# Optimization experiments

Hardware: AMD Instinct MI355X
Metric: run time of the kernel (lower is better)

The kernel has to match this reference:

```python
import jax, jax.numpy as jnp
import numpy as np

NUM_HEADS = 8
NUM_GROUPS = 32
EPS = 1e-5


def group_norm(x, gamma, beta):
    # x: (B, C, N)
    B, C, N = x.shape
    xg = x.reshape(B, NUM_GROUPS, (C // NUM_GROUPS) * N)
    mean = xg.mean(axis=-1, keepdims=True)
    var = xg.var(axis=-1, keepdims=True)
    xg = (xg - mean) * jax.lax.rsqrt(var + EPS)
    x = xg.reshape(B, C, N)
    return x * gamma[None, :, None] + beta[None, :, None]


def setup_inputs() -> dict:
    key = jax.random.key(0)
    ks = jax.random.split(key, 7)
    B, C, H, W = 16, 512, 32, 32
    return {
        "x": jax.random.normal(ks[0], (B, C, H, W), dtype=jnp.float32),
        "gamma": jax.random.uniform(ks[1], (C,), dtype=jnp.float32, minval=0.5, maxval=1.5),
        "beta": jax.random.normal(ks[2], (C,), dtype=jnp.float32) * 0.1,
        "w_qkv": jax.random.normal(ks[3], (3 * C, C), dtype=jnp.float32) * 0.02,
        "b_qkv": jax.random.normal(ks[4], (3 * C,), dtype=jnp.float32) * 0.01,
        "w_proj": jax.random.normal(ks[5], (C, C), dtype=jnp.float32) * 0.02,
        "b_proj": jax.random.normal(ks[6], (C,), dtype=jnp.float32) * 0.01,
    }


def reference(x, gamma, beta, w_qkv, b_qkv, w_proj, b_proj):
    B, C, Hs, Ws = x.shape
    N = Hs * Ws
    x3 = x.reshape(B, C, N)
    xn = group_norm(x3, gamma, beta)
    # 1x1 Conv1d == channel-wise linear: (3C, C) x (B, C, N) -> (B, 3C, N)
    qkv = jnp.einsum('oc,bcn->bon', w_qkv, xn) + b_qkv[None, :, None]
    ch = C // NUM_HEADS
    qkv = qkv.reshape(B * NUM_HEADS, 3 * ch, N)
    q, k, v = jnp.split(qkv, 3, axis=1)  # each (B*H, ch, N)
    scale = ch ** (-0.25)
    w = jnp.einsum('bct,bcs->bts', q * scale, k * scale)  # (B*H, N, N)
    w = jax.nn.softmax(w.astype(jnp.float32), axis=-1).astype(q.dtype)
    h = jnp.einsum('bts,bcs->bct', w, v)  # (B*H, ch, N)
    h = h.reshape(B, C, N)
    h = jnp.einsum('oc,bcn->bon', w_proj, h) + b_proj[None, :, None]
    return (x3 + h).reshape(B, C, Hs, Ws)
```

## Files before the change

kernel.cpp:

```cpp
#include <hip/hip_runtime.h>
#include <stdint.h>

typedef unsigned short u16;
typedef float f32x4 __attribute__((ext_vector_type(4)));
typedef short bf16x8 __attribute__((ext_vector_type(8)));

#define DEV __device__ __forceinline__

DEV u16 f2bf(float f) {
  union { float f; unsigned int u; } v; v.f = f;
  unsigned int u = v.u;
  u = (u + 0x7FFFu + ((u >> 16) & 1u)) >> 16;
  return (u16)u;
}

DEV float exp2_(float x) {
#if __has_builtin(__builtin_amdgcn_exp2f)
  return __builtin_amdgcn_exp2f(x);
#else
  return exp2f(x);
#endif
}

DEV unsigned int cvt_pk_bf16(float lo, float hi) {
  unsigned int r;
  asm("v_cvt_pk_bf16_f32 %0, %1, %2" : "=v"(r) : "v"(lo), "v"(hi));
  return r;
}

typedef __attribute__((address_space(1))) const unsigned int* gas_t;
typedef __attribute__((address_space(3))) unsigned int* las_t;
DEV void gload16(const void* g, void* l) {
  __builtin_amdgcn_global_load_lds((gas_t)g, (las_t)l, 16, 0, 0);
}

DEV f32x4 zf4() { f32x4 z = {0.f, 0.f, 0.f, 0.f}; return z; }

static constexpr float QK_SCALE = 0.35355339059327373f;
static constexpr float LOG2E    = 1.4426950408889634f;

static constexpr size_t OFF_WQKV  = 0;
static constexpr size_t OFF_WPROJ = 1572864;
static constexpr size_t OFF_XNT   = 2097152;
static constexpr size_t OFF_Q     = 18874368;
static constexpr size_t OFF_K     = 35651584;
static constexpr size_t OFF_V     = 52428800;
static constexpr size_t OFF_HT    = 69206016;

__global__ __launch_bounds__(256) void wconv_kernel(const float* __restrict__ wqkv,
                                                    const float* __restrict__ wproj,
                                                    u16* __restrict__ dq, u16* __restrict__ dp) {
  int i = blockIdx.x * 256 + threadIdx.x;
  const float4* src; u16* dst; int j;
  if (i < 196608) { src = (const float4*)wqkv;  dst = dq; j = i; }
  else            { src = (const float4*)wproj; dst = dp; j = i - 196608; }
  float4 v = src[j];
  unsigned int lo = (unsigned int)f2bf(v.x) | ((unsigned int)f2bf(v.y) << 16);
  unsigned int hi = (unsigned int)f2bf(v.z) | ((unsigned int)f2bf(v.w) << 16);
  uint2 o; o.x = lo; o.y = hi;
  *(uint2*)(dst + (size_t)j * 4) = o;
}

__global__ __launch_bounds__(256, 4) void gn_fused_kernel(const float* __restrict__ x,
                                                          const float* __restrict__ gamma,
                                                          const float* __restrict__ beta,
                                                          u16* __restrict__ xnt) {
  __shared__ u16 Tls[16 * 1024];
  __shared__ float rs[4], rss[4], bcast[2];
  int grp = blockIdx.x;
  int b = grp >> 5, g = grp & 31;
  int tid = threadIdx.x;
  const float4* p = (const float4*)(x + (size_t)grp * 16384);
  float4 v[16];
  float s = 0.f, ss = 0.f;
  #pragma unroll
  for (int it = 0; it < 16; ++it) {
    v[it] = p[it * 256 + tid];
    s  += v[it].x + v[it].y + v[it].z + v[it].w;
    ss += v[it].x*v[it].x + v[it].y*v[it].y + v[it].z*v[it].z + v[it].w*v[it].w;
  }
  #pragma unroll
  for (int off = 32; off > 0; off >>= 1) {
    s  += __shfl_down(s, off);
    ss += __shfl_down(ss, off);
  }
  int wid = tid >> 6;
  if ((tid & 63) == 0) { rs[wid] = s; rss[wid] = ss; }
  __syncthreads();
  if (tid == 0) {
    s  = rs[0] + rs[1] + rs[2] + rs[3];
    ss = rss[0] + rss[1] + rss[2] + rss[3];
    float mean = s * (1.f / 16384.f);
    float var  = ss * (1.f / 16384.f) - mean * mean;
    bcast[0] = mean;
    bcast[1] = rsqrtf(var + 1e-5f);
  }
  __syncthreads();
  float mean = bcast[0], rstd = bcast[1];
  #pragma unroll
  for (int it = 0; it < 16; ++it) {
    int c = g*16 + it;
    float ga = gamma[c] * rstd, be = beta[c] - mean * ga;
    uint2 pk;
    pk.x = cvt_pk_bf16(v[it].x*ga + be, v[it].y*ga + be);
    pk.y = cvt_pk_bf16(v[it].z*ga + be, v[it].w*ga + be);
    *(uint2*)&Tls[it*1024 + tid*4] = pk;
  }
  __syncthreads();
  u16* dst = xnt + ((size_t)b * 1024) * 512 + g*16;
  for (int r = 0; r < 8; ++r) {
    int idx = r*256 + tid, n = idx >> 1, half = idx & 1;
    u16 tmp[8];
    #pragma unroll
    for (int cc = 0; cc < 8; ++cc) tmp[cc] = Tls[(half*8 + cc)*1024 + n];
    *(uint4*)(dst + (size_t)n*512 + half*8) = *(uint4*)tmp;
  }
}

template<int EPI>
__global__ __launch_bounds__(256) void gemm_kernel(const u16* __restrict__ A,
                                                   const u16* __restrict__ Bm,
                                                   const float* __restrict__ bias,
                                                   u16* __restrict__ Qp, u16* __restrict__ Kp,
                                                   u16* __restrict__ Vp,
                                                   const float* __restrict__ xres,
                                                   float* __restrict__ outp) {
  __shared__ u16 lds[4 * 128 * 64];
  int tid = threadIdx.x, lane = tid & 63, wid = tid >> 6;
  int tl = lane & 15, g = lane >> 4;
  int wm = wid >> 1, wn = wid & 1;
  int tM = blockIdx.y, tN = blockIdx.x;
  int o0 = tM * 128, n0 = tN * 128;
  f32x4 acc[4][4];
  #pragma unroll
  for (int i = 0; i < 4; ++i)
    #pragma unroll
    for (int j = 0; j < 4; ++j) acc[i][j] = zf4();

  int rl = lane >> 3, sg = lane & 7;
  const u16* Ag = A  + (size_t)(o0 + wid*32 + rl) * 512 + ((sg ^ rl) << 3);
  const u16* Bg = Bm + (size_t)(n0 + wid*32 + rl) * 512 + ((sg ^ rl) << 3);
  int wofs = wid*32*64;

#define STAGE_GEMM(buf, kt)                                                     \
  {                                                                             \
    u16* Ad = lds + (buf)*16384 + wofs;                                         \
    u16* Bd = lds + (buf)*16384 + 8192 + wofs;                                  \
    _Pragma("unroll")                                                           \
    for (int q = 0; q < 4; ++q) {                                               \
      gload16(Ag + (size_t)q*8*512 + (kt)*64, Ad + q*8*64);                     \
      gload16(Bg + (size_t)q*8*512 + (kt)*64, Bd + q*8*64);                     \
    }                                                                           \
  }

  STAGE_GEMM(0, 0);
  __syncthreads();
  for (int kt = 0; kt < 8; ++kt) {
    int cur = kt & 1;
    if (kt < 7) STAGE_GEMM(cur ^ 1, kt + 1);
    const u16* Als = lds + cur*16384;
    const u16* Bls = lds + cur*16384 + 8192;
    #pragma unroll
    for (int kk = 0; kk < 2; ++kk) {
      bf16x8 av[4], bv[4];
      #pragma unroll
      for (int mi = 0; mi < 4; ++mi)
        av[mi] = *(const bf16x8*)&Als[(wm*64 + mi*16 + tl)*64 + (((kk*4 + g) ^ (tl & 7)) << 3)];
      #pragma unroll
      for (int ni = 0; ni < 4; ++ni)
        bv[ni] = *(const bf16x8*)&Bls[(wn*64 + ni*16 + tl)*64 + (((kk*4 + g) ^ (tl & 7)) << 3)];
      #pragma unroll
      for (int mi = 0; mi < 4; ++mi)
        #pragma unroll
        for (int ni = 0; ni < 4; ++ni)
          acc[mi][ni] = __builtin_amdgcn_mfma_f32_16x16x32_bf16(av[mi], bv[ni], acc[mi][ni], 0, 0, 0);
    }
    __syncthreads();
  }
#undef STAGE_GEMM

  if (EPI == 1) {
    #pragma unroll
    for (int mi = 0; mi < 4; ++mi) {
      int mb = mi*16 + (g << 2);
      float4 bs = *(const float4*)&bias[o0 + wm*64 + mb];
      const float* bsf = (const float*)&bs;
      #pragma unroll
      for (int ni = 0; ni < 4; ++ni) {
        int n_g = n0 + wn*64 + ni*16 + tl;
        int bb = n_g >> 10, n = n_g & 1023;
        #pragma unroll
        for (int rr = 0; rr < 4; ++rr) {
          int o_g = o0 + wm*64 + mb + rr;
          size_t oi = (((size_t)(bb*512 + o_g)) << 10) + n;
          outp[oi] = acc[mi][ni][rr] + bsf[rr] + xres[oi];
        }
      }
    }
    return;
  }

  int a = 2*tM + wm;
  int head = a / 3;
  int sect = a - head*3;
  float sc = (sect == 0) ? QK_SCALE : (sect == 1 ? QK_SCALE * LOG2E : 1.f);
  u16* wl = lds + wid * (64*64);
  #pragma unroll
  for (int mi = 0; mi < 4; ++mi) {
    int mb = mi*16 + (g << 2);
    float4 bs = *(const float4*)&bias[o0 + wm*64 + mb];
    const float* bsf = (const float*)&bs;
    #pragma unroll
    for (int ni = 0; ni < 4; ++ni) {
      int nl = ni*16 + tl;
      #pragma unroll
      for (int rr = 0; rr < 4; ++rr) {
        float val = (acc[mi][ni][rr] + bsf[rr]) * sc;
        int ml = mb + rr;
        if (sect < 2) wl[nl*64 + (ml ^ ((nl & 7) << 3))] = f2bf(val);
        else          wl[ml*64 + (nl ^ ((ml & 7) << 3))] = f2bf(val);
      }
    }
  }
  int n_wb = n0 + wn*64;
  int bb = n_wb >> 10, nn0 = n_wb & 1023;
  int bh = bb*8 + head;
  #pragma unroll
  for (int p = 0; p < 8; ++p) {
    int row = p*8 + (lane >> 3), sgg = lane & 7;
    uint4 v = *(const uint4*)&wl[row*64 + ((sgg ^ (row & 7)) << 3)];
    if (sect == 0)
      *(uint4*)(Qp + (((size_t)bh) << 16) + (size_t)(nn0 + row)*64 + sgg*8) = v;
    else if (sect == 1)
      *(uint4*)(Kp + (((size_t)bh) << 16) + (size_t)(nn0 + row)*64 + sgg*8) = v;
    else
      *(uint4*)(Vp + (((size_t)bh) << 16) + (size_t)row*1024 + nn0 + sgg*8) = v;
  }
}

__global__ __launch_bounds__(256, 4) void attn_kernel(const u16* __restrict__ Qp,
                                                      const u16* __restrict__ Kp,
                                                      const u16* __restrict__ Vp,
                                                      u16* __restrict__ Hp) {
  __shared__ u16 Kls[64 * 64];
  __shared__ u16 Vls[64 * 64];
  __shared__ u16 Pls[4 * 32 * 64];
  int tid = threadIdx.x, lane = tid & 63, w = tid >> 6;
  int id = blockIdx.x;
  int bh = ((id >> 6) << 3) | (id & 7);
  int tblk = (id >> 3) & 7;
  int t0 = tblk * 128 + w * 32;
  size_t hb = ((size_t)bh) << 16;
  int tl = lane & 15, g = lane >> 4;

  bf16x8 bq[2][2];
  #pragma unroll
  for (int tf = 0; tf < 2; ++tf)
    #pragma unroll
    for (int kk = 0; kk < 2; ++kk)
      bq[tf][kk] = *(const bf16x8*)(Qp + hb + (size_t)(t0 + tf*16 + tl)*64 + kk*32 + g*8);

  f32x4 oacc[4][2];
  #pragma unroll
  for (int ci = 0; ci < 4; ++ci)
    #pragma unroll
    for (int tf = 0; tf < 2; ++tf) oacc[ci][tf] = zf4();
  float l_run[2] = {0.f, 0.f};
  u16* pw = Pls + w * (32 * 64);
  int sr = tid >> 3, sseg = tid & 7;
  int xsw = (tl & 7) << 3;

  for (int s0 = 0; s0 < 1024; s0 += 64) {
    #pragma unroll
    for (int p = 0; p < 2; ++p) {
      int row = p*32 + sr;
      int woff = row*64 + ((sseg ^ (row & 7)) << 3);
      *(uint4*)&Kls[woff] = *(const uint4*)(Kp + hb + (size_t)(s0 + row)*64 + sseg*8);
      *(uint4*)&Vls[woff] = *(const uint4*)(Vp + hb + (size_t)row*1024 + s0 + sseg*8);
    }
    __syncthreads();

    f32x4 sfr[2][4];
    #pragma unroll
    for (int tf = 0; tf < 2; ++tf)
      #pragma unroll
      for (int ni = 0; ni < 4; ++ni) sfr[tf][ni] = zf4();
    __builtin_amdgcn_s_setprio(1);
    #pragma unroll
    for (int kk = 0; kk < 2; ++kk) {
      bf16x8 ak[4];
      #pragma unroll
      for (int ni = 0; ni < 4; ++ni)
        ak[ni] = *(const bf16x8*)&Kls[(ni*16 + tl)*64 + ((((kk*4 + g) << 3)) ^ xsw)];
      #pragma unroll
      for (int tf = 0; tf < 2; ++tf)
        #pragma unroll
        for (int ni = 0; ni < 4; ++ni)
          sfr[tf][ni] = __builtin_amdgcn_mfma_f32_16x16x32_bf16(ak[ni], bq[tf][kk], sfr[tf][ni], 0, 0, 0);
    }
    __builtin_amdgcn_s_setprio(0);

    #pragma unroll
    for (int tf = 0; tf < 2; ++tf) {
      int trow = tf*16 + tl;
      int rsw = (trow & 7) << 3;
      float lt = 0.f;
      #pragma unroll
      for (int ni = 0; ni < 4; ++ni) {
        float p0 = exp2_(sfr[tf][ni][0]);
        float p1 = exp2_(sfr[tf][ni][1]);
        float p2 = exp2_(sfr[tf][ni][2]);
        float p3 = exp2_(sfr[tf][ni][3]);
        lt += (p0 + p1) + (p2 + p3);
        uint2 pkv;
        pkv.x = cvt_pk_bf16(p0, p1);
        pkv.y = cvt_pk_bf16(p2, p3);
        *(uint2*)&pw[trow*64 + ((ni*16 + g*4) ^ rsw)] = pkv;
      }
      l_run[tf] += lt;
    }

    __builtin_amdgcn_s_setprio(1);
    #pragma unroll
    for (int kk = 0; kk < 2; ++kk) {
      bf16x8 av[4];
      #pragma unroll
      for (int ci = 0; ci < 4; ++ci)
        av[ci] = *(const bf16x8*)&Vls[(ci*16 + tl)*64 + ((((kk*4 + g) << 3)) ^ xsw)];
      #pragma unroll
      for (int tf = 0; tf < 2; ++tf) {
        int trow = tf*16 + tl;
        bf16x8 bp = *(const bf16x8*)&pw[trow*64 + (((kk*4 + g) << 3) ^ ((trow & 7) << 3))];
        #pragma unroll
        for (int ci = 0; ci < 4; ++ci)
          oacc[ci][tf] = __builtin_amdgcn_mfma_f32_16x16x32_bf16(av[ci], bp, oacc[ci][tf], 0, 0, 0);
      }
    }
    __builtin_amdgcn_s_setprio(0);
    __syncthreads();
  }

  #pragma unroll
  for (int tf = 0; tf < 2; ++tf) {
    float l = l_run[tf];
    l += __shfl_xor(l, 16);
    l += __shfl_xor(l, 32);
    float inv = 1.f / l;
    int trow = tf*16 + tl;
    int rsw = (trow & 7) << 3;
    #pragma unroll
    for (int ci = 0; ci < 4; ++ci) {
      uint2 pkv;
      pkv.x = cvt_pk_bf16(oacc[ci][tf][0]*inv, oacc[ci][tf][1]*inv);
      pkv.y = cvt_pk_bf16(oacc[ci][tf][2]*inv, oacc[ci][tf][3]*inv);
      *(uint2*)&pw[trow*64 + ((ci*16 + g*4) ^ rsw)] = pkv;
    }
  }
  int b = bh >> 3, head = bh & 7;
  #pragma unroll
  for (int p = 0; p < 4; ++p) {
    int row = p*8 + (lane >> 3), sgg = lane & 7;
    uint4 v = *(const uint4*)&pw[row*64 + ((sgg ^ (row & 7)) << 3)];
    *(uint4*)(Hp + ((size_t)(b*1024 + t0 + row))*512 + head*64 + sgg*8) = v;
  }
}

extern "C" void kernel_launch(void* const* d_in, const int* in_sizes, int n_in,
                              void* d_out, int out_size, void* d_ws, size_t ws_size,
                              hipStream_t stream) {
  const float* x     = (const float*)d_in[0];
  const float* gamma = (const float*)d_in[1];
  const float* beta  = (const float*)d_in[2];
  const float* wqkv  = (const float*)d_in[3];
  const float* bqkv  = (const float*)d_in[4];
  const float* wproj = (const float*)d_in[5];
  const float* bproj = (const float*)d_in[6];
  float* out = (float*)d_out;
  char* ws = (char*)d_ws;
  u16* wqkv_bf  = (u16*)(ws + OFF_WQKV);
  u16* wproj_bf = (u16*)(ws + OFF_WPROJ);
  u16* xnt = (u16*)(ws + OFF_XNT);
  u16* Qp  = (u16*)(ws + OFF_Q);
  u16* Kp  = (u16*)(ws + OFF_K);
  u16* Vp  = (u16*)(ws + OFF_V);
  u16* Hp  = (u16*)(ws + OFF_HT);

  wconv_kernel<<<1024, 256, 0, stream>>>(wqkv, wproj, wqkv_bf, wproj_bf);
  gn_fused_kernel<<<512, 256, 0, stream>>>(x, gamma, beta, xnt);
  gemm_kernel<0><<<dim3(128, 12), 256, 0, stream>>>(wqkv_bf, xnt, bqkv, Qp, Kp, Vp, nullptr, nullptr);
  attn_kernel<<<1024, 256, 0, stream>>>(Qp, Kp, Vp, Hp);
  gemm_kernel<1><<<dim3(128, 4), 256, 0, stream>>>(wproj_bf, Hp, bproj, nullptr, nullptr, nullptr, x, out);
}
```

Baseline: 194.5 us.

## Merge weight-convert and groupnorm kernels; double-buffer K/V with async LDS loads

Folds the weight bf16 conversion and the groupnorm kernel into one launch, with blocks split by index. The groupnorm transpose now writes straight from registers instead of staging through shared memory. Attention K/V tiles are double-buffered using global_load_lds direct-to-LDS loads, so the next tile's load overlaps compute on the current one and one sync per iteration is removed. This doubles K/V shared memory, which may lower occupancy, and the direct transposed stores are less coalesced.

```diff
diff --git a/kernel.cpp b/kernel.cpp
--- a/kernel.cpp
+++ b/kernel.cpp
@@ -47,30 +47,28 @@
 static constexpr size_t OFF_V     = 52428800;
 static constexpr size_t OFF_HT    = 69206016;
 
-__global__ __launch_bounds__(256) void wconv_kernel(const float* __restrict__ wqkv,
-                                                    const float* __restrict__ wproj,
-                                                    u16* __restrict__ dq, u16* __restrict__ dp) {
-  int i = blockIdx.x * 256 + threadIdx.x;
-  const float4* src; u16* dst; int j;
-  if (i < 196608) { src = (const float4*)wqkv;  dst = dq; j = i; }
-  else            { src = (const float4*)wproj; dst = dp; j = i - 196608; }
-  float4 v = src[j];
-  unsigned int lo = (unsigned int)f2bf(v.x) | ((unsigned int)f2bf(v.y) << 16);
-  unsigned int hi = (unsigned int)f2bf(v.z) | ((unsigned int)f2bf(v.w) << 16);
-  uint2 o; o.x = lo; o.y = hi;
-  *(uint2*)(dst + (size_t)j * 4) = o;
-}
-
-__global__ __launch_bounds__(256, 4) void gn_fused_kernel(const float* __restrict__ x,
-                                                          const float* __restrict__ gamma,
-                                                          const float* __restrict__ beta,
-                                                          u16* __restrict__ xnt) {
-  __shared__ u16 Tls[16 * 1024];
+__global__ __launch_bounds__(256) void prep_kernel(const float* __restrict__ x,
+                                                   const float* __restrict__ gamma,
+                                                   const float* __restrict__ beta,
+                                                   const float* __restrict__ wqkv,
+                                                   const float* __restrict__ wproj,
+                                                   u16* __restrict__ xnt,
+                                                   u16* __restrict__ dq, u16* __restrict__ dp) {
+  int tid = threadIdx.x;
+  int blk = blockIdx.x;
+  if (blk >= 512) {
+    int i = (blk - 512) * 256 + tid;
+    const float4* src; u16* dst; int j;
+    if (i < 196608) { src = (const float4*)wqkv;  dst = dq; j = i; }
+    else            { src = (const float4*)wproj; dst = dp; j = i - 196608; }
+    float4 v = src[j];
+    uint2 o; o.x = cvt_pk_bf16(v.x, v.y); o.y = cvt_pk_bf16(v.z, v.w);
+    *(uint2*)(dst + (size_t)j * 4) = o;
+    return;
+  }
   __shared__ float rs[4], rss[4], bcast[2];
-  int grp = blockIdx.x;
-  int b = grp >> 5, g = grp & 31;
-  int tid = threadIdx.x;
-  const float4* p = (const float4*)(x + (size_t)grp * 16384);
+  int b = blk >> 5, g = blk & 31;
+  const float4* p = (const float4*)(x + (size_t)blk * 16384);
   float4 v[16];
   float s = 0.f, ss = 0.f;
   #pragma unroll
@@ -97,23 +95,32 @@
   }
   __syncthreads();
   float mean = bcast[0], rstd = bcast[1];
+  float ga[16], be[16];
   #pragma unroll
   for (int it = 0; it < 16; ++it) {
-    int c = g*16 + it;
-    float ga = gamma[c] * rstd, be = beta[c] - mean * ga;
-    uint2 pk;
-    pk.x = cvt_pk_bf16(v[it].x*ga + be, v[it].y*ga + be);
-    pk.y = cvt_pk_bf16(v[it].z*ga + be, v[it].w*ga + be);
-    *(uint2*)&Tls[it*1024 + tid*4] = pk;
-  }
-  __syncthreads();
-  u16* dst = xnt + ((size_t)b * 1024) * 512 + g*16;
-  for (int r = 0; r < 8; ++r) {
-    int idx = r*256 + tid, n = idx >> 1, half = idx & 1;
-    u16 tmp[8];
-    #pragma unroll
-    for (int cc = 0; cc < 8; ++cc) tmp[cc] = Tls[(half*8 + cc)*1024 + n];
-    *(uint4*)(dst + (size_t)n*512 + half*8) = *(uint4*)tmp;
+    float gm = gamma[g*16 + it];
+    ga[it] = gm * rstd;
+    be[it] = beta[g*16 + it] - mean * ga[it];
+  }
+  u16* dst = xnt + ((size_t)(b*1024 + tid*4)) * 512 + g*16;
+  #pragma unroll
+  for (int k = 0; k < 4; ++k) {
+    unsigned int w[8];
+    #pragma unroll
+    for (int j = 0; j < 8; ++j) {
+      float e, o;
+      switch (k) {
+        case 0: e = v[2*j].x; o = v[2*j+1].x; break;
+        case 1: e = v[2*j].y; o = v[2*j+1].y; break;
+        case 2: e = v[2*j].z; o = v[2*j+1].z; break;
+        default: e = v[2*j].w; o = v[2*j+1].w; break;
+      }
+      w[j] = cvt_pk_bf16(e*ga[2*j] + be[2*j], o*ga[2*j+1] + be[2*j+1]);
+    }
+    uint4 lo; lo.x = w[0]; lo.y = w[1]; lo.z = w[2]; lo.w = w[3];
+    uint4 hi; hi.x = w[4]; hi.y = w[5]; hi.z = w[6]; hi.w = w[7];
+    *(uint4*)(dst + (size_t)k*512)     = lo;
+    *(uint4*)(dst + (size_t)k*512 + 8) = hi;
   }
 }
 
@@ -242,8 +249,7 @@
                                                       const u16* __restrict__ Kp,
                                                       const u16* __restrict__ Vp,
                                                       u16* __restrict__ Hp) {
-  __shared__ u16 Kls[64 * 64];
-  __shared__ u16 Vls[64 * 64];
+  __shared__ u16 KVls[2 * 2 * 4096];
   __shared__ u16 Pls[4 * 32 * 64];
   int tid = threadIdx.x, lane = tid & 63, w = tid >> 6;
   int id = blockIdx.x;
@@ -267,18 +273,28 @@
     for (int tf = 0; tf < 2; ++tf) oacc[ci][tf] = zf4();
   float l_run[2] = {0.f, 0.f};
   u16* pw = Pls + w * (32 * 64);
-  int sr = tid >> 3, sseg = tid & 7;
   int xsw = (tl & 7) << 3;
 
-  for (int s0 = 0; s0 < 1024; s0 += 64) {
-    #pragma unroll
-    for (int p = 0; p < 2; ++p) {
-      int row = p*32 + sr;
-      int woff = row*64 + ((sseg ^ (row & 7)) << 3);
-      *(uint4*)&Kls[woff] = *(const uint4*)(Kp + hb + (size_t)(s0 + row)*64 + sseg*8);
-      *(uint4*)&Vls[woff] = *(const uint4*)(Vp + hb + (size_t)row*1024 + s0 + sseg*8);
-    }
-    __syncthreads();
+  int r8 = lane >> 3, sg8 = lane & 7;
+  int swz = ((sg8 ^ r8) << 3);
+
+#define STAGE_KV(buf, sbase)                                                        \
+  { _Pragma("unroll")                                                               \
+    for (int q = 0; q < 2; ++q) {                                                   \
+      int row = q*32 + w*8 + r8;                                                    \
+      gload16(Kp + hb + (size_t)(sbase + row)*64 + swz,                             \
+              KVls + (buf)*8192 + (q*256 + w*64)*8);                                \
+      gload16(Vp + hb + (size_t)row*1024 + (sbase) + swz,                           \
+              KVls + (buf)*8192 + 4096 + (q*256 + w*64)*8);                         \
+    } }
+
+  STAGE_KV(0, 0);
+  __syncthreads();
+  for (int it = 0; it < 16; ++it) {
+    int cur = it & 1;
+    if (it < 15) STAGE_KV(cur ^ 1, (it + 1) * 64);
+    const u16* Kls = KVls + cur*8192;
+    const u16* Vls = KVls + cur*8192 + 4096;
 
     f32x4 sfr[2][4];
     #pragma unroll
@@ -339,6 +355,7 @@
     __builtin_amdgcn_s_setprio(0);
     __syncthreads();
   }
+#undef STAGE_KV
 
   #pragma unroll
   for (int tf = 0; tf < 2; ++tf) {
@@ -385,8 +402,7 @@
   u16* Vp  = (u16*)(ws + OFF_V);
   u16* Hp  = (u16*)(ws + OFF_HT);
 
-  wconv_kernel<<<1024, 256, 0, stream>>>(wqkv, wproj, wqkv_bf, wproj_bf);
-  gn_fused_kernel<<<512, 256, 0, stream>>>(x, gamma, beta, xnt);
+  prep_kernel<<<1536, 256, 0, stream>>>(x, gamma, beta, wqkv, wproj, xnt, wqkv_bf, wproj_bf);
   gemm_kernel<0><<<dim3(128, 12), 256, 0, stream>>>(wqkv_bf, xnt, bqkv, Qp, Kp, Vp, nullptr, nullptr);
   attn_kernel<<<1024, 256, 0, stream>>>(Qp, Kp, Vp, Hp);
   gemm_kernel<1><<<dim3(128, 4), 256, 0, stream>>>(wproj_bf, Hp, bproj, nullptr, nullptr, nullptr, x, out);
```

Result: slower. 204.3 us (+5.0%).
